# Optimization experiments

Measured on AMD Instinct MI355X. Metric: run time of the kernel, lower is better.

## Reference

```python
import jax, jax.numpy as jnp
import numpy as np

B, C, L = 4, 512, 2048
CI = 512          # inter_channels (must equal num_heads*head_dim)
H, D = 8, 64      # num_heads, head_dim = C // H
EPS = 1e-5        # BatchNorm1d eps


def setup_inputs() -> dict:
    key = jax.random.key(0)
    ks = jax.random.split(key, 9)
    s_in = 1.0 / np.sqrt(C)
    s_ci = 1.0 / np.sqrt(CI)
    return {
        "x": jax.random.normal(ks[0], (B, C, L), dtype=jnp.float32),
        "g_w": jax.random.uniform(ks[1], (CI, C), jnp.float32, -s_in, s_in),
        "g_b": jax.random.uniform(ks[2], (CI,), jnp.float32, -s_in, s_in),
        "theta_w": jax.random.uniform(ks[3], (CI, C), jnp.float32, -s_in, s_in),
        "theta_b": jax.random.uniform(ks[4], (CI,), jnp.float32, -s_in, s_in),
        "phi_w": jax.random.uniform(ks[5], (CI, C), jnp.float32, -s_in, s_in),
        "phi_b": jax.random.uniform(ks[6], (CI,), jnp.float32, -s_in, s_in),
        "w_w": jax.random.uniform(ks[7], (C, CI), jnp.float32, -s_ci, s_ci),
        "w_b": jax.random.uniform(ks[8], (C,), jnp.float32, -s_ci, s_ci),
        # BN affine params (torch inits them to 0, which zeroes the output;
        # use random values so the reference output / grads are non-trivial)
        "bn_gamma": jax.random.normal(jax.random.fold_in(key, 10), (C,), jnp.float32),
        "bn_beta": jax.random.normal(jax.random.fold_in(key, 11), (C,), jnp.float32),
    }


def _conv1x1(w, b, x):
    # x: [B, Cin, L], w: [Cout, Cin] -> [B, Cout, L]
    return jnp.einsum("oc,bcl->bol", w, x) + b[None, :, None]


def reference(x, g_w, g_b, theta_w, theta_b, phi_w, phi_b, w_w, w_b, bn_gamma, bn_beta):
    b, _, l = x.shape
    # 1x1 conv projections, split into heads: [B, H, D, L]
    g_x = _conv1x1(g_w, g_b, x).reshape(b, H, D, l).transpose(0, 1, 3, 2)      # [B,H,L,D]
    theta_x = _conv1x1(theta_w, theta_b, x).reshape(b, H, D, l).transpose(0, 1, 3, 2)  # [B,H,L,D]
    phi_x = _conv1x1(phi_w, phi_b, x).reshape(b, H, D, l)                       # [B,H,D,L]

    scale = 1.0 / jnp.sqrt(jnp.asarray(D, dtype=x.dtype))
    scores = jnp.einsum("bhqd,bhdk->bhqk", theta_x, phi_x) * scale  # [B,H,L,L]
    attn = jax.nn.softmax(scores, axis=-1)
    y = jnp.einsum("bhqk,bhkd->bhqd", attn, g_x)                    # [B,H,L,D]
    y = y.transpose(0, 1, 3, 2).reshape(b, CI, l)                   # [B,CI,L]

    # W: 1x1 conv + BatchNorm1d (training mode, biased batch stats)
    wy = _conv1x1(w_w, w_b, y)                                      # [B,C,L]
    mean = jnp.mean(wy, axis=(0, 2), keepdims=True)
    var = jnp.mean((wy - mean) ** 2, axis=(0, 2), keepdims=True)
    wy_hat = (wy - mean) * jax.lax.rsqrt(var + EPS)
    return wy_hat * bn_gamma[None, :, None] + bn_beta[None, :, None]
```

## Files before the change

### kernel.cpp

```cpp
#include <hip/hip_runtime.h>

constexpr int Bn = 4, Cn = 512, Ln = 2048, CIn = 512, Hn = 8, Dn = 64;
constexpr int COn = 3 * CIn;

typedef unsigned short u16;
typedef unsigned int u32;
typedef __attribute__((ext_vector_type(8))) short bfrag;
typedef __attribute__((ext_vector_type(4))) float facc;

#define SCF 0.180336879f

__device__ __forceinline__ facc mfma16(bfrag a, bfrag b, facc c) {
  return __builtin_amdgcn_mfma_f32_16x16x32_bf16(a, b, c, 0, 0, 0);
}

__device__ __forceinline__ void async16(const void* g, void* l) {
  __builtin_amdgcn_global_load_lds((const __attribute__((address_space(1))) void*)g,
                                   (__attribute__((address_space(3))) void*)l, 16, 0, 0);
}

__device__ __forceinline__ u16 f2bf(float x) {
  union { float f; u32 u; } v; v.f = x;
  u32 r = v.u + 0x7FFFu + ((v.u >> 16) & 1u);
  return (u16)(r >> 16);
}

__device__ __forceinline__ u16 f2bf_fast(float x) {
  union { float f; u32 u; } v; v.f = x;
  return (u16)((v.u + 0x8000u) >> 16);
}

__device__ __forceinline__ u32 pkbf(float lof, float hif) {
  union { float f; u32 u; } a, b; a.f = lof; b.f = hif;
  return __builtin_amdgcn_perm(b.u + 0x8000u, a.u + 0x8000u, 0x07060302u);
}

__device__ __forceinline__ float bflo(u32 u) { return __uint_as_float(u << 16); }
__device__ __forceinline__ float bfhi(u32 u) { return __uint_as_float(u & 0xFFFF0000u); }

__device__ __forceinline__ bfrag fr8(const u16* base, int row, int gi) {
  return *(const bfrag*)&base[row * 64 + ((gi ^ (row & 7)) * 8)];
}

__global__ void k_misc(const float* __restrict__ x, const float* __restrict__ gw,
                       const float* __restrict__ tw, const float* __restrict__ pw,
                       const float* __restrict__ ww, u16* __restrict__ xT,
                       u16* __restrict__ Wcat, u16* __restrict__ Ww,
                       float* __restrict__ stats) {
  int b = blockIdx.z;
  if (b == 4) {
    int i = (blockIdx.y * 64 + blockIdx.x) * 256 + threadIdx.x;
    if (i < CIn * Cn) {
      Wcat[i]                = f2bf(tw[i] * SCF);
      Wcat[CIn * Cn + i]     = f2bf(pw[i]);
      Wcat[2 * CIn * Cn + i] = f2bf(gw[i]);
      Ww[i]                  = f2bf(ww[i]);
    }
    if (i < 2 * Cn) stats[i] = 0.f;
    return;
  }
  __shared__ float tile[32][33];
  int l0 = blockIdx.x * 32, c0 = blockIdx.y * 32;
  int tx = threadIdx.x & 31, ty = threadIdx.x >> 5;
  const float* xb = x + (size_t)b * Cn * Ln;
  for (int k = 0; k < 4; k++)
    tile[ty + k * 8][tx] = xb[(size_t)(c0 + ty + k * 8) * Ln + l0 + tx];
  __syncthreads();
  u16* xtb = xT + (size_t)b * Ln * Cn;
  int cc = (threadIdx.x & 15) * 2, r0 = threadIdx.x >> 4;
  for (int k = 0; k < 2; k++) {
    int ll = r0 + k * 16;
    u32 pk = pkbf(tile[cc][ll], tile[cc + 1][ll]);
    *(u32*)&xtb[(size_t)(l0 + ll) * Cn + c0 + cc] = pk;
  }
}

__device__ __forceinline__ void stage128x32(const u16* g, int K, int k0, u16* lds,
                                            int w, int l) {
  int gsw = ((l & 3) ^ ((l >> 3) & 3)) * 8;
  for (int jj = 0; jj < 2; jj++) {
    int j = w * 2 + jj;
    const u16* ga = g + (size_t)(j * 16 + (l >> 2)) * K + k0 + gsw;
    async16(ga, (char*)lds + j * 1024 + l * 16);
  }
}

__device__ __forceinline__ void gemm_core(const u16* A, const u16* Bt, int K,
                                          u16* As, u16* Bs, facc acc[4][4],
                                          int w, int l) {
  int quad = l >> 4, lo = l & 15;
  int mw = (w >> 1) * 64, nw = (w & 1) * 64;
  int rsw = (lo >> 1) & 3;
  for (int k0 = 0; k0 < K; k0 += 32) {
    stage128x32(A, K, k0, As, w, l);
    stage128x32(Bt, K, k0, Bs, w, l);
    __syncthreads();
    bfrag af[4], bfv[4];
    for (int mi = 0; mi < 4; mi++)
      af[mi] = *(const bfrag*)&As[(mw + mi * 16 + lo) * 32 + ((quad ^ rsw) * 8)];
    for (int ni = 0; ni < 4; ni++)
      bfv[ni] = *(const bfrag*)&Bs[(nw + ni * 16 + lo) * 32 + ((quad ^ rsw) * 8)];
    for (int mi = 0; mi < 4; mi++)
      for (int ni = 0; ni < 4; ni++)
        acc[mi][ni] = mfma16(af[mi], bfv[ni], acc[mi][ni]);
    __syncthreads();
  }
}

__device__ __forceinline__ void gemm_core64(const u16* A, const u16* Bt, int K,
                                            u16* As, u16* Bs, facc acc[2][4],
                                            int w, int l) {
  int quad = l >> 4, lo = l & 15;
  int mw = (w >> 1) * 32, nw = (w & 1) * 64;
  int rsw = (lo >> 1) & 3;
  int gsw = ((l & 3) ^ ((l >> 3) & 3)) * 8;
  for (int k0 = 0; k0 < K; k0 += 32) {
    async16(A + (size_t)(w * 16 + (l >> 2)) * K + k0 + gsw, (char*)As + w * 1024 + l * 16);
    stage128x32(Bt, K, k0, Bs, w, l);
    __syncthreads();
    bfrag af[2], bfv[4];
    for (int mi = 0; mi < 2; mi++)
      af[mi] = *(const bfrag*)&As[(mw + mi * 16 + lo) * 32 + ((quad ^ rsw) * 8)];
    for (int ni = 0; ni < 4; ni++)
      bfv[ni] = *(const bfrag*)&Bs[(nw + ni * 16 + lo) * 32 + ((quad ^ rsw) * 8)];
    for (int mi = 0; mi < 2; mi++)
      for (int ni = 0; ni < 4; ni++)
        acc[mi][ni] = mfma16(af[mi], bfv[ni], acc[mi][ni]);
    __syncthreads();
  }
}

__global__ __launch_bounds__(256) void k_proj(
    const u16* __restrict__ Wcat, const u16* __restrict__ xT,
    const float* __restrict__ tb, const float* __restrict__ pb,
    const float* __restrict__ gb, u16* __restrict__ Q, u16* __restrict__ Kb,
    u16* __restrict__ Vt) {
  __shared__ __align__(16) u16 As[128 * 32];
  __shared__ __align__(16) u16 Bs[128 * 32];
  int w = threadIdx.x >> 6, l = threadIdx.x & 63;
  int quad = l >> 4, lo = l & 15;
  int m0 = blockIdx.y * 128, n0 = blockIdx.x * 128, b = blockIdx.z;
  facc acc[4][4] = {};
  gemm_core(Wcat + (size_t)m0 * Cn, xT + ((size_t)b * Ln + n0) * Cn, Cn, As, Bs, acc, w, l);
  int mw = (w >> 1) * 64, nw = (w & 1) * 64;
  int chunk = m0 >> 9;
  for (int mi = 0; mi < 4; mi++) {
    int mo = (m0 + mw + mi * 16) & 511;
    int hh = mo >> 6;
    int db = (mo & 63) + quad * 4;
    int bi = mo + quad * 4;
    if (chunk < 2) {
      const float* bias = (chunk == 0) ? tb : pb;
      float bs = (chunk == 0) ? SCF : 1.0f;
      u16* dst0 = ((chunk == 0) ? Q : Kb) + (size_t)(b * Hn + hh) * Ln * 64 + db;
      float b0 = bias[bi] * bs, b1 = bias[bi + 1] * bs;
      float b2 = bias[bi + 2] * bs, b3 = bias[bi + 3] * bs;
      for (int ni = 0; ni < 4; ni++) {
        int lcol = n0 + nw + ni * 16 + lo;
        facc a = acc[mi][ni];
        uint2 pk;
        pk.x = pkbf(a[0] + b0, a[1] + b1);
        pk.y = pkbf(a[2] + b2, a[3] + b3);
        *(uint2*)(dst0 + (size_t)lcol * 64) = pk;
      }
    } else {
      for (int ni = 0; ni < 4; ni++) {
        int lcol = n0 + nw + ni * 16 + lo;
        facc a = acc[mi][ni];
        for (int r = 0; r < 4; r++)
          Vt[((size_t)(b * Hn + hh) * Dn + db + r) * Ln + lcol] = f2bf_fast(a[r] + gb[bi + r]);
      }
    }
  }
}

__global__ __launch_bounds__(256, 2) void k_attn(
    const u16* __restrict__ Q, const u16* __restrict__ Kb,
    const u16* __restrict__ Vt, u16* __restrict__ Opart,
    float* __restrict__ lpart) {
  __shared__ __align__(16) u16 lds[24576];
  u16* Ks = lds;
  u16* Vs = lds + 8192;
  u16* QPs = lds + 16384;
  int w = threadIdx.x >> 6, l = threadIdx.x & 63;
  int quad = l >> 4, lo = l & 15;
  int q0 = blockIdx.x * 128, h = blockIdx.y >> 1, split = blockIdx.y & 1, b = blockIdx.z;
  size_t bh = (size_t)b * Hn + h;
  const u16* Qg = Q + bh * Ln * 64;
  const u16* Kg = Kb + bh * Ln * 64 + (size_t)split * 1024 * 64;
  const u16* Vg = Vt + bh * (size_t)Dn * Ln + split * 1024;

  int rin = l >> 3;
  int gg = ((l & 7) ^ rin) * 8;

  for (int jj = 0; jj < 4; jj++) {
    int j = w * 4 + jj;
    async16(Qg + (size_t)(q0 + j * 8 + rin) * 64 + gg, (char*)QPs + j * 1024 + l * 16);
  }
  for (int jj = 0; jj < 2; jj++) {
    int j = w * 2 + jj;
    async16(Kg + (size_t)(j * 8 + rin) * 64 + gg, (char*)Ks + j * 1024 + l * 16);
    async16(Vg + (size_t)(j * 8 + rin) * Ln + gg, (char*)Vs + j * 1024 + l * 16);
  }
  __syncthreads();
  bfrag qf[2][2];
  for (int s = 0; s < 2; s++)
    for (int c = 0; c < 2; c++)
      qf[s][c] = fr8(QPs, w * 32 + s * 16 + lo, c * 4 + quad);

  facc o[2][4] = {};
  float l_i[2] = {0.f, 0.f};

  for (int t = 0; t < 16; t++) {
    const u16* Kc = Ks + (t & 1) * 4096;
    const u16* Vc = Vs + (t & 1) * 4096;
    if (t < 15) {
      int nb = (~t & 1) * 4096;
      int kbase = (t + 1) * 64;
      for (int jj = 0; jj < 2; jj++) {
        int j = w * 2 + jj;
        async16(Kg + (size_t)(kbase + j * 8 + rin) * 64 + gg,
                (char*)(Ks + nb) + j * 1024 + l * 16);
        async16(Vg + (size_t)(j * 8 + rin) * Ln + kbase + gg,
                (char*)(Vs + nb) + j * 1024 + l * 16);
      }
    }
    for (int ni = 0; ni < 4; ni++) {
      bfrag kf0 = fr8(Kc, ni * 16 + lo, quad);
      bfrag kf1 = fr8(Kc, ni * 16 + lo, 4 + quad);
      for (int s = 0; s < 2; s++) {
        facc z = {};
        facc stv = mfma16(kf1, qf[s][1], mfma16(kf0, qf[s][0], z));
        float p0 = __builtin_amdgcn_exp2f(stv[0]);
        float p1 = __builtin_amdgcn_exp2f(stv[1]);
        float p2 = __builtin_amdgcn_exp2f(stv[2]);
        float p3 = __builtin_amdgcn_exp2f(stv[3]);
        l_i[s] += (p0 + p1) + (p2 + p3);
        int row = w * 32 + s * 16 + lo;
        uint2 pk;
        pk.x = pkbf(p0, p1);
        pk.y = pkbf(p2, p3);
        int gi = ni * 2 + (quad >> 1);
        *(uint2*)&QPs[row * 64 + ((gi ^ (row & 7)) * 8) + (quad & 1) * 4] = pk;
      }
    }
    bfrag pb2[2][2];
    for (int s = 0; s < 2; s++)
      for (int c = 0; c < 2; c++)
        pb2[s][c] = fr8(QPs, w * 32 + s * 16 + lo, c * 4 + quad);
    for (int mi = 0; mi < 4; mi++) {
      bfrag vf0 = fr8(Vc, mi * 16 + lo, quad);
      bfrag vf1 = fr8(Vc, mi * 16 + lo, 4 + quad);
      for (int s = 0; s < 2; s++)
        o[s][mi] = mfma16(vf1, pb2[s][1], mfma16(vf0, pb2[s][0], o[s][mi]));
    }
    __syncthreads();
  }
  int sb = split * 32 + (int)bh;
  for (int s = 0; s < 2; s++) {
    float lt = l_i[s];
    lt += __shfl_xor(lt, 16);
    lt += __shfl_xor(lt, 32);
    int q = q0 + w * 32 + s * 16 + lo;
    u16* dst = Opart + ((size_t)sb * Ln + q) * 64;
    for (int mi = 0; mi < 4; mi++) {
      uint2 pk;
      pk.x = pkbf(o[s][mi][0], o[s][mi][1]);
      pk.y = pkbf(o[s][mi][2], o[s][mi][3]);
      *(uint2*)(dst + mi * 16 + quad * 4) = pk;
    }
    if (quad == 0) lpart[(size_t)sb * Ln + q] = lt;
  }
}

__global__ void k_comb(const u16* __restrict__ Opart, const float* __restrict__ lpart,
                       u16* __restrict__ yT) {
  int i = blockIdx.x * 256 + threadIdx.x;
  int bhq = i >> 3, d0 = (i & 7) * 8;
  int bh = bhq >> 11, q = bhq & 2047;
  const u16* o1 = Opart + ((size_t)bh * Ln + q) * 64 + d0;
  const u16* o2 = o1 + (size_t)32 * Ln * 64;
  float inv = 1.0f / (lpart[bhq] + lpart[65536 + bhq]);
  uint4 a = *(const uint4*)o1, c = *(const uint4*)o2;
  uint4 r;
  r.x = pkbf((bflo(a.x) + bflo(c.x)) * inv, (bfhi(a.x) + bfhi(c.x)) * inv);
  r.y = pkbf((bflo(a.y) + bflo(c.y)) * inv, (bfhi(a.y) + bfhi(c.y)) * inv);
  r.z = pkbf((bflo(a.z) + bflo(c.z)) * inv, (bfhi(a.z) + bfhi(c.z)) * inv);
  r.w = pkbf((bflo(a.w) + bflo(c.w)) * inv, (bfhi(a.w) + bfhi(c.w)) * inv);
  int b = bh >> 3, h = bh & 7;
  *(uint4*)(yT + ((size_t)b * Ln + q) * CIn + h * 64 + d0) = r;
}

__global__ __launch_bounds__(256) void k_wgemm(
    const u16* __restrict__ Ww, const u16* __restrict__ yT,
    const float* __restrict__ wb, u16* __restrict__ wy,
    float* __restrict__ stats) {
  __shared__ __align__(16) u16 As[64 * 32];
  __shared__ __align__(16) u16 Bs[128 * 32];
  int w = threadIdx.x >> 6, l = threadIdx.x & 63;
  int quad = l >> 4, lo = l & 15;
  int m0 = blockIdx.y * 64, n0 = blockIdx.x * 128, b = blockIdx.z;
  facc acc[2][4] = {};
  gemm_core64(Ww + (size_t)m0 * CIn, yT + ((size_t)b * Ln + n0) * CIn, CIn, As, Bs, acc, w, l);
  int mw = (w >> 1) * 32, nw = (w & 1) * 64;
  for (int mi = 0; mi < 2; mi++) {
    int cb = m0 + mw + mi * 16 + quad * 4;
    for (int r = 0; r < 4; r++) {
      float bias = wb[cb + r];
      float s = 0.f, q = 0.f;
      for (int ni = 0; ni < 4; ni++) {
        float v = acc[mi][ni][r] + bias;
        wy[((size_t)b * Cn + cb + r) * Ln + n0 + nw + ni * 16 + lo] = f2bf_fast(v);
        s += v; q += v * v;
      }
      for (int mask = 1; mask < 16; mask <<= 1) {
        s += __shfl_xor(s, mask);
        q += __shfl_xor(q, mask);
      }
      if (lo == 0) {
        atomicAdd(&stats[cb + r], s);
        atomicAdd(&stats[Cn + cb + r], q);
      }
    }
  }
}

__global__ void k_bn(const u16* __restrict__ wy, const float* __restrict__ stats,
                     const float* __restrict__ gam, const float* __restrict__ bet,
                     float* __restrict__ out) {
  int i = blockIdx.x * 256 + threadIdx.x;
  size_t idx = (size_t)i * 8;
  int c = (int)((idx >> 11) & (Cn - 1));
  const float invN = 1.f / (Bn * Ln);
  float mean = stats[c] * invN;
  float var = stats[Cn + c] * invN - mean * mean;
  float scl = gam[c] * rsqrtf(var + 1e-5f);
  float sh = bet[c] - mean * scl;
  uint4 v = *(const uint4*)(wy + idx);
  float4 o0, o1;
  o0.x = bflo(v.x) * scl + sh; o0.y = bfhi(v.x) * scl + sh;
  o0.z = bflo(v.y) * scl + sh; o0.w = bfhi(v.y) * scl + sh;
  o1.x = bflo(v.z) * scl + sh; o1.y = bfhi(v.z) * scl + sh;
  o1.z = bflo(v.w) * scl + sh; o1.w = bfhi(v.w) * scl + sh;
  *(float4*)(out + idx) = o0;
  *(float4*)(out + idx + 4) = o1;
}

extern "C" void kernel_launch(void* const* d_in, const int* in_sizes, int n_in,
                              void* d_out, int out_size, void* d_ws, size_t ws_size,
                              hipStream_t stream) {
  const float* x   = (const float*)d_in[0];
  const float* g_w = (const float*)d_in[1];
  const float* g_b = (const float*)d_in[2];
  const float* t_w = (const float*)d_in[3];
  const float* t_b = (const float*)d_in[4];
  const float* p_w = (const float*)d_in[5];
  const float* p_b = (const float*)d_in[6];
  const float* w_w = (const float*)d_in[7];
  const float* w_b = (const float*)d_in[8];
  const float* gam = (const float*)d_in[9];
  const float* bet = (const float*)d_in[10];
  float* out = (float*)d_out;

  char* ws = (char*)d_ws;
  size_t off = 0;
  auto alloc = [&](size_t bytes) {
    char* p = ws + off; off += (bytes + 255) & ~(size_t)255; return p;
  };
  u16*  xT   = (u16*)alloc((size_t)Bn * Ln * Cn * 2);
  u16*  Wcat = (u16*)alloc((size_t)COn * Cn * 2);
  u16*  Ww   = (u16*)alloc((size_t)Cn * CIn * 2);
  u16*  Qb   = (u16*)alloc((size_t)Bn * Hn * Ln * Dn * 2);
  u16*  Kb   = (u16*)alloc((size_t)Bn * Hn * Ln * Dn * 2);
  u16*  Vt   = (u16*)alloc((size_t)Bn * Hn * Dn * Ln * 2);
  u16*  yT   = (u16*)alloc((size_t)Bn * Ln * CIn * 2);
  size_t opart_bytes = (size_t)2 * 32 * Ln * 64 * 2;
  u16*  Opart = (u16*)alloc(opart_bytes);
  u16*  wy    = Opart;
  float* lpart = (float*)alloc((size_t)2 * 32 * Ln * 4);
  float* st  = (float*)alloc(2 * Cn * 4);
  if (ws_size < off) return;

  k_misc<<<dim3(64, 16, 5), 256, 0, stream>>>(x, g_w, t_w, p_w, w_w, xT, Wcat, Ww, st);
  k_proj<<<dim3(16, 12, 4), 256, 0, stream>>>(Wcat, xT, t_b, p_b, g_b, Qb, Kb, Vt);
  k_attn<<<dim3(16, 16, 4), 256, 0, stream>>>(Qb, Kb, Vt, Opart, lpart);
  k_comb<<<dim3(2048), 256, 0, stream>>>(Opart, lpart, yT);
  k_wgemm<<<dim3(16, 8, 4), 256, 0, stream>>>(Ww, yT, w_b, wy, st);
  k_bn<<<dim3(2048), 256, 0, stream>>>(wy, st, gam, bet, out);
}
```

Baseline: 195.5 us.

## Fuse split-KV combine into attention via atomic counter, halve KV tile size

The attention kernel now processes 32-key tiles instead of 64, halving LDS use so four blocks can be resident per CU, as the new launch bound requests. The separate combine kernel is removed. Each block writes its partial output, and whichever of the two split blocks finishes last, detected with a global atomic counter and fences, reads the other split's partial and writes the normalized result to yT. This saves a kernel launch and one pass over the partials, at the cost of doubling the loop iterations and barriers and adding fence and atomic overhead.

```diff
diff --git a/kernel.cpp b/kernel.cpp
--- a/kernel.cpp
+++ b/kernel.cpp
@@ -40,6 +40,9 @@
 
 __device__ __forceinline__ bfrag fr8(const u16* base, int row, int gi) {
   return *(const bfrag*)&base[row * 64 + ((gi ^ (row & 7)) * 8)];
+}
+__device__ __forceinline__ bfrag fr4(const u16* base, int row, int gi) {
+  return *(const bfrag*)&base[row * 32 + ((gi ^ (row & 3)) * 8)];
 }
 
 __global__ void k_misc(const float* __restrict__ x, const float* __restrict__ gw,
@@ -56,7 +59,7 @@
       Wcat[2 * CIn * Cn + i] = f2bf(gw[i]);
       Ww[i]                  = f2bf(ww[i]);
     }
-    if (i < 2 * Cn) stats[i] = 0.f;
+    if (i < 2 * Cn + 512) stats[i] = 0.f;
     return;
   }
   __shared__ float tile[32][33];
@@ -174,14 +177,15 @@
   }
 }
 
-__global__ __launch_bounds__(256, 2) void k_attn(
+__global__ __launch_bounds__(256, 4) void k_attn(
     const u16* __restrict__ Q, const u16* __restrict__ Kb,
     const u16* __restrict__ Vt, u16* __restrict__ Opart,
-    float* __restrict__ lpart) {
-  __shared__ __align__(16) u16 lds[24576];
+    float* __restrict__ lpart, int* __restrict__ cnt, u16* __restrict__ yT) {
+  __shared__ __align__(16) u16 lds[16384];
+  __shared__ int sOld;
   u16* Ks = lds;
-  u16* Vs = lds + 8192;
-  u16* QPs = lds + 16384;
+  u16* Vs = lds + 4096;
+  u16* QPs = lds + 8192;
   int w = threadIdx.x >> 6, l = threadIdx.x & 63;
   int quad = l >> 4, lo = l & 15;
   int q0 = blockIdx.x * 128, h = blockIdx.y >> 1, split = blockIdx.y & 1, b = blockIdx.z;
@@ -192,16 +196,14 @@
 
   int rin = l >> 3;
   int gg = ((l & 7) ^ rin) * 8;
+  int ggv = ((l & 3) ^ ((l >> 2) & 3)) * 8;
 
   for (int jj = 0; jj < 4; jj++) {
     int j = w * 4 + jj;
     async16(Qg + (size_t)(q0 + j * 8 + rin) * 64 + gg, (char*)QPs + j * 1024 + l * 16);
   }
-  for (int jj = 0; jj < 2; jj++) {
-    int j = w * 2 + jj;
-    async16(Kg + (size_t)(j * 8 + rin) * 64 + gg, (char*)Ks + j * 1024 + l * 16);
-    async16(Vg + (size_t)(j * 8 + rin) * Ln + gg, (char*)Vs + j * 1024 + l * 16);
-  }
+  async16(Kg + (size_t)(w * 8 + rin) * 64 + gg, (char*)Ks + w * 1024 + l * 16);
+  async16(Vg + (size_t)(w * 16 + (l >> 2)) * Ln + ggv, (char*)Vs + w * 1024 + l * 16);
   __syncthreads();
   bfrag qf[2][2];
   for (int s = 0; s < 2; s++)
@@ -211,21 +213,18 @@
   facc o[2][4] = {};
   float l_i[2] = {0.f, 0.f};
 
-  for (int t = 0; t < 16; t++) {
-    const u16* Kc = Ks + (t & 1) * 4096;
-    const u16* Vc = Vs + (t & 1) * 4096;
-    if (t < 15) {
-      int nb = (~t & 1) * 4096;
-      int kbase = (t + 1) * 64;
-      for (int jj = 0; jj < 2; jj++) {
-        int j = w * 2 + jj;
-        async16(Kg + (size_t)(kbase + j * 8 + rin) * 64 + gg,
-                (char*)(Ks + nb) + j * 1024 + l * 16);
-        async16(Vg + (size_t)(j * 8 + rin) * Ln + kbase + gg,
-                (char*)(Vs + nb) + j * 1024 + l * 16);
-      }
-    }
-    for (int ni = 0; ni < 4; ni++) {
+  for (int t = 0; t < 32; t++) {
+    const u16* Kc = Ks + (t & 1) * 2048;
+    const u16* Vc = Vs + (t & 1) * 2048;
+    if (t < 31) {
+      int nb = (~t & 1) * 2048;
+      int kbase = (t + 1) * 32;
+      async16(Kg + (size_t)(kbase + w * 8 + rin) * 64 + gg,
+              (char*)(Ks + nb) + w * 1024 + l * 16);
+      async16(Vg + (size_t)(w * 16 + (l >> 2)) * Ln + kbase + ggv,
+              (char*)(Vs + nb) + w * 1024 + l * 16);
+    }
+    for (int ni = 0; ni < 2; ni++) {
       bfrag kf0 = fr8(Kc, ni * 16 + lo, quad);
       bfrag kf1 = fr8(Kc, ni * 16 + lo, 4 + quad);
       for (int s = 0; s < 2; s++) {
@@ -244,23 +243,24 @@
         *(uint2*)&QPs[row * 64 + ((gi ^ (row & 7)) * 8) + (quad & 1) * 4] = pk;
       }
     }
-    bfrag pb2[2][2];
+    bfrag pb2[2];
     for (int s = 0; s < 2; s++)
-      for (int c = 0; c < 2; c++)
-        pb2[s][c] = fr8(QPs, w * 32 + s * 16 + lo, c * 4 + quad);
+      pb2[s] = fr8(QPs, w * 32 + s * 16 + lo, quad);
     for (int mi = 0; mi < 4; mi++) {
-      bfrag vf0 = fr8(Vc, mi * 16 + lo, quad);
-      bfrag vf1 = fr8(Vc, mi * 16 + lo, 4 + quad);
+      bfrag vf = fr4(Vc, mi * 16 + lo, quad);
       for (int s = 0; s < 2; s++)
-        o[s][mi] = mfma16(vf1, pb2[s][1], mfma16(vf0, pb2[s][0], o[s][mi]));
-    }
-    __syncthreads();
-  }
+        o[s][mi] = mfma16(vf, pb2[s], o[s][mi]);
+    }
+    __syncthreads();
+  }
+
   int sb = split * 32 + (int)bh;
+  float lt[2];
   for (int s = 0; s < 2; s++) {
-    float lt = l_i[s];
-    lt += __shfl_xor(lt, 16);
-    lt += __shfl_xor(lt, 32);
+    float v = l_i[s];
+    v += __shfl_xor(v, 16);
+    v += __shfl_xor(v, 32);
+    lt[s] = v;
     int q = q0 + w * 32 + s * 16 + lo;
     u16* dst = Opart + ((size_t)sb * Ln + q) * 64;
     for (int mi = 0; mi < 4; mi++) {
@@ -269,26 +269,29 @@
       pk.y = pkbf(o[s][mi][2], o[s][mi][3]);
       *(uint2*)(dst + mi * 16 + quad * 4) = pk;
     }
-    if (quad == 0) lpart[(size_t)sb * Ln + q] = lt;
-  }
-}
-
-__global__ void k_comb(const u16* __restrict__ Opart, const float* __restrict__ lpart,
-                       u16* __restrict__ yT) {
-  int i = blockIdx.x * 256 + threadIdx.x;
-  int bhq = i >> 3, d0 = (i & 7) * 8;
-  int bh = bhq >> 11, q = bhq & 2047;
-  const u16* o1 = Opart + ((size_t)bh * Ln + q) * 64 + d0;
-  const u16* o2 = o1 + (size_t)32 * Ln * 64;
-  float inv = 1.0f / (lpart[bhq] + lpart[65536 + bhq]);
-  uint4 a = *(const uint4*)o1, c = *(const uint4*)o2;
-  uint4 r;
-  r.x = pkbf((bflo(a.x) + bflo(c.x)) * inv, (bfhi(a.x) + bfhi(c.x)) * inv);
-  r.y = pkbf((bflo(a.y) + bflo(c.y)) * inv, (bfhi(a.y) + bfhi(c.y)) * inv);
-  r.z = pkbf((bflo(a.z) + bflo(c.z)) * inv, (bfhi(a.z) + bfhi(c.z)) * inv);
-  r.w = pkbf((bflo(a.w) + bflo(c.w)) * inv, (bfhi(a.w) + bfhi(c.w)) * inv);
-  int b = bh >> 3, h = bh & 7;
-  *(uint4*)(yT + ((size_t)b * Ln + q) * CIn + h * 64 + d0) = r;
+    if (quad == 0) lpart[(size_t)sb * Ln + q] = lt[s];
+  }
+  __threadfence();
+  __syncthreads();
+  if (threadIdx.x == 0)
+    sOld = atomicAdd(cnt + ((int)bh * 16 + blockIdx.x), 1);
+  __syncthreads();
+  if (sOld == 0) return;
+  __threadfence();
+  int sbo = (1 - split) * 32 + (int)bh;
+  for (int s = 0; s < 2; s++) {
+    int q = q0 + w * 32 + s * 16 + lo;
+    const u16* osrc = Opart + ((size_t)sbo * Ln + q) * 64;
+    float inv = 1.0f / (lt[s] + lpart[(size_t)sbo * Ln + q]);
+    u16* dst = yT + ((size_t)b * Ln + q) * CIn + h * 64;
+    for (int mi = 0; mi < 4; mi++) {
+      uint2 ov = *(const uint2*)(osrc + mi * 16 + quad * 4);
+      uint2 pk;
+      pk.x = pkbf((o[s][mi][0] + bflo(ov.x)) * inv, (o[s][mi][1] + bfhi(ov.x)) * inv);
+      pk.y = pkbf((o[s][mi][2] + bflo(ov.y)) * inv, (o[s][mi][3] + bfhi(ov.y)) * inv);
+      *(uint2*)(dst + mi * 16 + quad * 4) = pk;
+    }
+  }
 }
 
 __global__ __launch_bounds__(256) void k_wgemm(
@@ -378,13 +381,13 @@
   u16*  Opart = (u16*)alloc(opart_bytes);
   u16*  wy    = Opart;
   float* lpart = (float*)alloc((size_t)2 * 32 * Ln * 4);
-  float* st  = (float*)alloc(2 * Cn * 4);
+  float* st  = (float*)alloc((2 * Cn + 512) * 4);
+  int*  cnt  = (int*)(st + 2 * Cn);
   if (ws_size < off) return;
 
   k_misc<<<dim3(64, 16, 5), 256, 0, stream>>>(x, g_w, t_w, p_w, w_w, xT, Wcat, Ww, st);
   k_proj<<<dim3(16, 12, 4), 256, 0, stream>>>(Wcat, xT, t_b, p_b, g_b, Qb, Kb, Vt);
-  k_attn<<<dim3(16, 16, 4), 256, 0, stream>>>(Qb, Kb, Vt, Opart, lpart);
-  k_comb<<<dim3(2048), 256, 0, stream>>>(Opart, lpart, yT);
+  k_attn<<<dim3(16, 16, 4), 256, 0, stream>>>(Qb, Kb, Vt, Opart, lpart, cnt, yT);
   k_wgemm<<<dim3(16, 8, 4), 256, 0, stream>>>(Ww, yT, w_b, wy, st);
   k_bn<<<dim3(2048), 256, 0, stream>>>(wy, st, gam, bet, out);
 }
```

After: 382.9 us. +95.8%, slower.

## Fuse split-KV combine into W-GEMM loader and vectorize V-transpose stores

Applied to the files above, without the earlier changes.

Removes the separate combine kernel by having the W-projection GEMM read both attention partial outputs and their softmax denominators, normalize them, and write bf16 directly into its shared-memory B tile. This drops one launch and the yT round trip through global memory. The cost is synchronous global loads in the GEMM main loop in place of async LDS loads, with the combine work repeated across the 8 M-tile blocks. Separately, the V projection swaps the MFMA operands so each lane holds consecutive sequence positions and can emit packed 8-byte stores instead of scalar 2-byte scattered writes. wy is given its own buffer instead of aliasing Opart.

```diff
diff --git a/kernel.cpp b/kernel.cpp
--- a/kernel.cpp
+++ b/kernel.cpp
@@ -85,6 +85,7 @@
   }
 }
 
+template <int SWAP>
 __device__ __forceinline__ void gemm_core(const u16* A, const u16* Bt, int K,
                                           u16* As, u16* Bs, facc acc[4][4],
                                           int w, int l) {
@@ -102,30 +103,8 @@
       bfv[ni] = *(const bfrag*)&Bs[(nw + ni * 16 + lo) * 32 + ((quad ^ rsw) * 8)];
     for (int mi = 0; mi < 4; mi++)
       for (int ni = 0; ni < 4; ni++)
-        acc[mi][ni] = mfma16(af[mi], bfv[ni], acc[mi][ni]);
-    __syncthreads();
-  }
-}
-
-__device__ __forceinline__ void gemm_core64(const u16* A, const u16* Bt, int K,
-                                            u16* As, u16* Bs, facc acc[2][4],
-                                            int w, int l) {
-  int quad = l >> 4, lo = l & 15;
-  int mw = (w >> 1) * 32, nw = (w & 1) * 64;
-  int rsw = (lo >> 1) & 3;
-  int gsw = ((l & 3) ^ ((l >> 3) & 3)) * 8;
-  for (int k0 = 0; k0 < K; k0 += 32) {
-    async16(A + (size_t)(w * 16 + (l >> 2)) * K + k0 + gsw, (char*)As + w * 1024 + l * 16);
-    stage128x32(Bt, K, k0, Bs, w, l);
-    __syncthreads();
-    bfrag af[2], bfv[4];
-    for (int mi = 0; mi < 2; mi++)
-      af[mi] = *(const bfrag*)&As[(mw + mi * 16 + lo) * 32 + ((quad ^ rsw) * 8)];
-    for (int ni = 0; ni < 4; ni++)
-      bfv[ni] = *(const bfrag*)&Bs[(nw + ni * 16 + lo) * 32 + ((quad ^ rsw) * 8)];
-    for (int mi = 0; mi < 2; mi++)
-      for (int ni = 0; ni < 4; ni++)
-        acc[mi][ni] = mfma16(af[mi], bfv[ni], acc[mi][ni]);
+        acc[mi][ni] = SWAP ? mfma16(bfv[ni], af[mi], acc[mi][ni])
+                           : mfma16(af[mi], bfv[ni], acc[mi][ni]);
     __syncthreads();
   }
 }
@@ -140,18 +119,20 @@
   int w = threadIdx.x >> 6, l = threadIdx.x & 63;
   int quad = l >> 4, lo = l & 15;
   int m0 = blockIdx.y * 128, n0 = blockIdx.x * 128, b = blockIdx.z;
+  int chunk = m0 >> 9;
   facc acc[4][4] = {};
-  gemm_core(Wcat + (size_t)m0 * Cn, xT + ((size_t)b * Ln + n0) * Cn, Cn, As, Bs, acc, w, l);
+  const u16* Ap = Wcat + (size_t)m0 * Cn;
+  const u16* Bp = xT + ((size_t)b * Ln + n0) * Cn;
   int mw = (w >> 1) * 64, nw = (w & 1) * 64;
-  int chunk = m0 >> 9;
-  for (int mi = 0; mi < 4; mi++) {
-    int mo = (m0 + mw + mi * 16) & 511;
-    int hh = mo >> 6;
-    int db = (mo & 63) + quad * 4;
-    int bi = mo + quad * 4;
-    if (chunk < 2) {
-      const float* bias = (chunk == 0) ? tb : pb;
-      float bs = (chunk == 0) ? SCF : 1.0f;
+  if (chunk < 2) {
+    gemm_core<0>(Ap, Bp, Cn, As, Bs, acc, w, l);
+    const float* bias = (chunk == 0) ? tb : pb;
+    float bs = (chunk == 0) ? SCF : 1.0f;
+    for (int mi = 0; mi < 4; mi++) {
+      int mo = (m0 + mw + mi * 16) & 511;
+      int hh = mo >> 6;
+      int db = (mo & 63) + quad * 4;
+      int bi = mo + quad * 4;
       u16* dst0 = ((chunk == 0) ? Q : Kb) + (size_t)(b * Hn + hh) * Ln * 64 + db;
       float b0 = bias[bi] * bs, b1 = bias[bi + 1] * bs;
       float b2 = bias[bi + 2] * bs, b3 = bias[bi + 3] * bs;
@@ -163,12 +144,21 @@
         pk.y = pkbf(a[2] + b2, a[3] + b3);
         *(uint2*)(dst0 + (size_t)lcol * 64) = pk;
       }
-    } else {
+    }
+  } else {
+    gemm_core<1>(Ap, Bp, Cn, As, Bs, acc, w, l);
+    for (int mi = 0; mi < 4; mi++) {
+      int ch = (m0 + mw + mi * 16 + lo) & 511;
+      int hh = ch >> 6, d = ch & 63;
+      float bias = gb[ch];
+      u16* dst0 = Vt + ((size_t)(b * Hn + hh) * Dn + d) * Ln;
       for (int ni = 0; ni < 4; ni++) {
-        int lcol = n0 + nw + ni * 16 + lo;
+        int l0 = n0 + nw + ni * 16 + quad * 4;
         facc a = acc[mi][ni];
-        for (int r = 0; r < 4; r++)
-          Vt[((size_t)(b * Hn + hh) * Dn + db + r) * Ln + lcol] = f2bf_fast(a[r] + gb[bi + r]);
+        uint2 pk;
+        pk.x = pkbf(a[0] + bias, a[1] + bias);
+        pk.y = pkbf(a[2] + bias, a[3] + bias);
+        *(uint2*)(dst0 + l0) = pk;
       }
     }
   }
@@ -273,36 +263,58 @@
   }
 }
 
-__global__ void k_comb(const u16* __restrict__ Opart, const float* __restrict__ lpart,
-                       u16* __restrict__ yT) {
-  int i = blockIdx.x * 256 + threadIdx.x;
-  int bhq = i >> 3, d0 = (i & 7) * 8;
-  int bh = bhq >> 11, q = bhq & 2047;
-  const u16* o1 = Opart + ((size_t)bh * Ln + q) * 64 + d0;
-  const u16* o2 = o1 + (size_t)32 * Ln * 64;
-  float inv = 1.0f / (lpart[bhq] + lpart[65536 + bhq]);
-  uint4 a = *(const uint4*)o1, c = *(const uint4*)o2;
-  uint4 r;
-  r.x = pkbf((bflo(a.x) + bflo(c.x)) * inv, (bfhi(a.x) + bfhi(c.x)) * inv);
-  r.y = pkbf((bflo(a.y) + bflo(c.y)) * inv, (bfhi(a.y) + bfhi(c.y)) * inv);
-  r.z = pkbf((bflo(a.z) + bflo(c.z)) * inv, (bfhi(a.z) + bfhi(c.z)) * inv);
-  r.w = pkbf((bflo(a.w) + bflo(c.w)) * inv, (bfhi(a.w) + bfhi(c.w)) * inv);
-  int b = bh >> 3, h = bh & 7;
-  *(uint4*)(yT + ((size_t)b * Ln + q) * CIn + h * 64 + d0) = r;
-}
-
 __global__ __launch_bounds__(256) void k_wgemm(
-    const u16* __restrict__ Ww, const u16* __restrict__ yT,
-    const float* __restrict__ wb, u16* __restrict__ wy,
-    float* __restrict__ stats) {
+    const u16* __restrict__ Ww, const u16* __restrict__ Opart,
+    const float* __restrict__ lpart, const float* __restrict__ wb,
+    u16* __restrict__ wy, float* __restrict__ stats) {
   __shared__ __align__(16) u16 As[64 * 32];
   __shared__ __align__(16) u16 Bs[128 * 32];
-  int w = threadIdx.x >> 6, l = threadIdx.x & 63;
+  int tid = threadIdx.x;
+  int w = tid >> 6, l = tid & 63;
   int quad = l >> 4, lo = l & 15;
   int m0 = blockIdx.y * 64, n0 = blockIdx.x * 128, b = blockIdx.z;
+  const u16* A = Ww + (size_t)m0 * CIn;
   facc acc[2][4] = {};
-  gemm_core64(Ww + (size_t)m0 * CIn, yT + ((size_t)b * Ln + n0) * CIn, CIn, As, Bs, acc, w, l);
+  int gsw = ((l & 3) ^ ((l >> 3) & 3)) * 8;
+  int rsw = (lo >> 1) & 3;
   int mw = (w >> 1) * 32, nw = (w & 1) * 64;
+  int row = tid >> 1;
+  int rg = n0 + row;
+  int half = tid & 1;
+  int ssw = (row >> 1) & 3;
+  for (int k0 = 0; k0 < CIn; k0 += 32) {
+    async16(A + (size_t)(w * 16 + (l >> 2)) * CIn + k0 + gsw,
+            (char*)As + w * 1024 + l * 16);
+    int h = k0 >> 6;
+    int sb0 = b * 8 + h;
+    const u16* p1 = Opart + ((size_t)sb0 * Ln + rg) * 64 + (k0 & 63) + half * 16;
+    const u16* p2 = p1 + (size_t)32 * Ln * 64;
+    float inv = 1.0f / (lpart[(size_t)sb0 * Ln + rg] +
+                        lpart[(size_t)(sb0 + 32) * Ln + rg]);
+    uint4 a1 = *(const uint4*)p1, c1 = *(const uint4*)p2;
+    uint4 a2 = *(const uint4*)(p1 + 8), c2 = *(const uint4*)(p2 + 8);
+    uint4 r1, r2;
+    r1.x = pkbf((bflo(a1.x) + bflo(c1.x)) * inv, (bfhi(a1.x) + bfhi(c1.x)) * inv);
+    r1.y = pkbf((bflo(a1.y) + bflo(c1.y)) * inv, (bfhi(a1.y) + bfhi(c1.y)) * inv);
+    r1.z = pkbf((bflo(a1.z) + bflo(c1.z)) * inv, (bfhi(a1.z) + bfhi(c1.z)) * inv);
+    r1.w = pkbf((bflo(a1.w) + bflo(c1.w)) * inv, (bfhi(a1.w) + bfhi(c1.w)) * inv);
+    r2.x = pkbf((bflo(a2.x) + bflo(c2.x)) * inv, (bfhi(a2.x) + bfhi(c2.x)) * inv);
+    r2.y = pkbf((bflo(a2.y) + bflo(c2.y)) * inv, (bfhi(a2.y) + bfhi(c2.y)) * inv);
+    r2.z = pkbf((bflo(a2.z) + bflo(c2.z)) * inv, (bfhi(a2.z) + bfhi(c2.z)) * inv);
+    r2.w = pkbf((bflo(a2.w) + bflo(c2.w)) * inv, (bfhi(a2.w) + bfhi(c2.w)) * inv);
+    *(uint4*)&Bs[row * 32 + (((half * 2) ^ ssw) * 8)] = r1;
+    *(uint4*)&Bs[row * 32 + (((half * 2 + 1) ^ ssw) * 8)] = r2;
+    __syncthreads();
+    bfrag af[2], bfv[4];
+    for (int mi = 0; mi < 2; mi++)
+      af[mi] = *(const bfrag*)&As[(mw + mi * 16 + lo) * 32 + ((quad ^ rsw) * 8)];
+    for (int ni = 0; ni < 4; ni++)
+      bfv[ni] = *(const bfrag*)&Bs[(nw + ni * 16 + lo) * 32 + ((quad ^ rsw) * 8)];
+    for (int mi = 0; mi < 2; mi++)
+      for (int ni = 0; ni < 4; ni++)
+        acc[mi][ni] = mfma16(af[mi], bfv[ni], acc[mi][ni]);
+    __syncthreads();
+  }
   for (int mi = 0; mi < 2; mi++) {
     int cb = m0 + mw + mi * 16 + quad * 4;
     for (int r = 0; r < 4; r++) {
@@ -373,18 +385,15 @@
   u16*  Qb   = (u16*)alloc((size_t)Bn * Hn * Ln * Dn * 2);
   u16*  Kb   = (u16*)alloc((size_t)Bn * Hn * Ln * Dn * 2);
   u16*  Vt   = (u16*)alloc((size_t)Bn * Hn * Dn * Ln * 2);
-  u16*  yT   = (u16*)alloc((size_t)Bn * Ln * CIn * 2);
-  size_t opart_bytes = (size_t)2 * 32 * Ln * 64 * 2;
-  u16*  Opart = (u16*)alloc(opart_bytes);
-  u16*  wy    = Opart;
+  u16*  Opart = (u16*)alloc((size_t)2 * 32 * Ln * 64 * 2);
   float* lpart = (float*)alloc((size_t)2 * 32 * Ln * 4);
+  u16*  wy   = (u16*)alloc((size_t)Bn * Cn * Ln * 2);
   float* st  = (float*)alloc(2 * Cn * 4);
   if (ws_size < off) return;
 
   k_misc<<<dim3(64, 16, 5), 256, 0, stream>>>(x, g_w, t_w, p_w, w_w, xT, Wcat, Ww, st);
   k_proj<<<dim3(16, 12, 4), 256, 0, stream>>>(Wcat, xT, t_b, p_b, g_b, Qb, Kb, Vt);
   k_attn<<<dim3(16, 16, 4), 256, 0, stream>>>(Qb, Kb, Vt, Opart, lpart);
-  k_comb<<<dim3(2048), 256, 0, stream>>>(Opart, lpart, yT);
-  k_wgemm<<<dim3(16, 8, 4), 256, 0, stream>>>(Ww, yT, w_b, wy, st);
+  k_wgemm<<<dim3(16, 8, 4), 256, 0, stream>>>(Ww, Opart, lpart, w_b, wy, st);
   k_bn<<<dim3(2048), 256, 0, stream>>>(wy, st, gam, bet, out);
 }
```

Measured after the change: 196.1 us. Within noise of the previous version (+0.3%).

## Split attention keys three ways and vectorize transposed V projection stores

Applied to the files above, without the earlier changes.

The attention kernel now splits the 32 key tiles into three chunks (11/11/10) instead of two halves. This raises the grid from 1024 to 1536 blocks so the MI355X's CUs are better filled, and the combine kernel sums three partials. The V projection swaps the MFMA operand order so each lane holds contiguous sequence positions, allowing packed 8-byte stores into Vt instead of scattered 2-byte stores. The workspace is rearranged so yT and wy reuse the Q/K buffers, which keeps memory use in check with the larger partial buffers, at the cost of more partial-output traffic in the combine step.

```diff
diff --git a/kernel.cpp b/kernel.cpp
--- a/kernel.cpp
+++ b/kernel.cpp
@@ -85,6 +85,7 @@
   }
 }
 
+template <int SWAP>
 __device__ __forceinline__ void gemm_core(const u16* A, const u16* Bt, int K,
                                           u16* As, u16* Bs, facc acc[4][4],
                                           int w, int l) {
@@ -102,7 +103,8 @@
       bfv[ni] = *(const bfrag*)&Bs[(nw + ni * 16 + lo) * 32 + ((quad ^ rsw) * 8)];
     for (int mi = 0; mi < 4; mi++)
       for (int ni = 0; ni < 4; ni++)
-        acc[mi][ni] = mfma16(af[mi], bfv[ni], acc[mi][ni]);
+        acc[mi][ni] = SWAP ? mfma16(bfv[ni], af[mi], acc[mi][ni])
+                           : mfma16(af[mi], bfv[ni], acc[mi][ni]);
     __syncthreads();
   }
 }
@@ -140,18 +142,20 @@
   int w = threadIdx.x >> 6, l = threadIdx.x & 63;
   int quad = l >> 4, lo = l & 15;
   int m0 = blockIdx.y * 128, n0 = blockIdx.x * 128, b = blockIdx.z;
+  int chunk = m0 >> 9;
   facc acc[4][4] = {};
-  gemm_core(Wcat + (size_t)m0 * Cn, xT + ((size_t)b * Ln + n0) * Cn, Cn, As, Bs, acc, w, l);
+  const u16* Ap = Wcat + (size_t)m0 * Cn;
+  const u16* Bp = xT + ((size_t)b * Ln + n0) * Cn;
   int mw = (w >> 1) * 64, nw = (w & 1) * 64;
-  int chunk = m0 >> 9;
-  for (int mi = 0; mi < 4; mi++) {
-    int mo = (m0 + mw + mi * 16) & 511;
-    int hh = mo >> 6;
-    int db = (mo & 63) + quad * 4;
-    int bi = mo + quad * 4;
-    if (chunk < 2) {
-      const float* bias = (chunk == 0) ? tb : pb;
-      float bs = (chunk == 0) ? SCF : 1.0f;
+  if (chunk < 2) {
+    gemm_core<0>(Ap, Bp, Cn, As, Bs, acc, w, l);
+    const float* bias = (chunk == 0) ? tb : pb;
+    float bs = (chunk == 0) ? SCF : 1.0f;
+    for (int mi = 0; mi < 4; mi++) {
+      int mo = (m0 + mw + mi * 16) & 511;
+      int hh = mo >> 6;
+      int db = (mo & 63) + quad * 4;
+      int bi = mo + quad * 4;
       u16* dst0 = ((chunk == 0) ? Q : Kb) + (size_t)(b * Hn + hh) * Ln * 64 + db;
       float b0 = bias[bi] * bs, b1 = bias[bi + 1] * bs;
       float b2 = bias[bi + 2] * bs, b3 = bias[bi + 3] * bs;
@@ -163,12 +167,21 @@
         pk.y = pkbf(a[2] + b2, a[3] + b3);
         *(uint2*)(dst0 + (size_t)lcol * 64) = pk;
       }
-    } else {
+    }
+  } else {
+    gemm_core<1>(Ap, Bp, Cn, As, Bs, acc, w, l);
+    for (int mi = 0; mi < 4; mi++) {
+      int ch = (m0 + mw + mi * 16 + lo) & 511;
+      int hh = ch >> 6, d = ch & 63;
+      float bias = gb[ch];
+      u16* dst0 = Vt + ((size_t)(b * Hn + hh) * Dn + d) * Ln;
       for (int ni = 0; ni < 4; ni++) {
-        int lcol = n0 + nw + ni * 16 + lo;
+        int l0 = n0 + nw + ni * 16 + quad * 4;
         facc a = acc[mi][ni];
-        for (int r = 0; r < 4; r++)
-          Vt[((size_t)(b * Hn + hh) * Dn + db + r) * Ln + lcol] = f2bf_fast(a[r] + gb[bi + r]);
+        uint2 pk;
+        pk.x = pkbf(a[0] + bias, a[1] + bias);
+        pk.y = pkbf(a[2] + bias, a[3] + bias);
+        *(uint2*)(dst0 + l0) = pk;
       }
     }
   }
@@ -184,11 +197,14 @@
   u16* QPs = lds + 16384;
   int w = threadIdx.x >> 6, l = threadIdx.x & 63;
   int quad = l >> 4, lo = l & 15;
-  int q0 = blockIdx.x * 128, h = blockIdx.y >> 1, split = blockIdx.y & 1, b = blockIdx.z;
+  int q0 = blockIdx.x * 128, b = blockIdx.z;
+  int h = blockIdx.y / 3, split = blockIdx.y - h * 3;
+  int ts = split * 11;
+  int nt = (split == 2) ? 10 : 11;
   size_t bh = (size_t)b * Hn + h;
   const u16* Qg = Q + bh * Ln * 64;
-  const u16* Kg = Kb + bh * Ln * 64 + (size_t)split * 1024 * 64;
-  const u16* Vg = Vt + bh * (size_t)Dn * Ln + split * 1024;
+  const u16* Kg = Kb + bh * Ln * 64 + (size_t)ts * 4096;
+  const u16* Vg = Vt + bh * (size_t)Dn * Ln + ts * 64;
 
   int rin = l >> 3;
   int gg = ((l & 7) ^ rin) * 8;
@@ -211,10 +227,10 @@
   facc o[2][4] = {};
   float l_i[2] = {0.f, 0.f};
 
-  for (int t = 0; t < 16; t++) {
+  for (int t = 0; t < nt; t++) {
     const u16* Kc = Ks + (t & 1) * 4096;
     const u16* Vc = Vs + (t & 1) * 4096;
-    if (t < 15) {
+    if (t < nt - 1) {
       int nb = (~t & 1) * 4096;
       int kbase = (t + 1) * 64;
       for (int jj = 0; jj < 2; jj++) {
@@ -280,13 +296,18 @@
   int bh = bhq >> 11, q = bhq & 2047;
   const u16* o1 = Opart + ((size_t)bh * Ln + q) * 64 + d0;
   const u16* o2 = o1 + (size_t)32 * Ln * 64;
-  float inv = 1.0f / (lpart[bhq] + lpart[65536 + bhq]);
-  uint4 a = *(const uint4*)o1, c = *(const uint4*)o2;
+  const u16* o3 = o2 + (size_t)32 * Ln * 64;
+  float inv = 1.0f / (lpart[bhq] + lpart[65536 + bhq] + lpart[131072 + bhq]);
+  uint4 a = *(const uint4*)o1, c = *(const uint4*)o2, e = *(const uint4*)o3;
   uint4 r;
-  r.x = pkbf((bflo(a.x) + bflo(c.x)) * inv, (bfhi(a.x) + bfhi(c.x)) * inv);
-  r.y = pkbf((bflo(a.y) + bflo(c.y)) * inv, (bfhi(a.y) + bfhi(c.y)) * inv);
-  r.z = pkbf((bflo(a.z) + bflo(c.z)) * inv, (bfhi(a.z) + bfhi(c.z)) * inv);
-  r.w = pkbf((bflo(a.w) + bflo(c.w)) * inv, (bfhi(a.w) + bfhi(c.w)) * inv);
+  r.x = pkbf((bflo(a.x) + bflo(c.x) + bflo(e.x)) * inv,
+             (bfhi(a.x) + bfhi(c.x) + bfhi(e.x)) * inv);
+  r.y = pkbf((bflo(a.y) + bflo(c.y) + bflo(e.y)) * inv,
+             (bfhi(a.y) + bfhi(c.y) + bfhi(e.y)) * inv);
+  r.z = pkbf((bflo(a.z) + bflo(c.z) + bflo(e.z)) * inv,
+             (bfhi(a.z) + bfhi(c.z) + bfhi(e.z)) * inv);
+  r.w = pkbf((bflo(a.w) + bflo(c.w) + bflo(e.w)) * inv,
+             (bfhi(a.w) + bfhi(c.w) + bfhi(e.w)) * inv);
   int b = bh >> 3, h = bh & 7;
   *(uint4*)(yT + ((size_t)b * Ln + q) * CIn + h * 64 + d0) = r;
 }
@@ -373,17 +394,16 @@
   u16*  Qb   = (u16*)alloc((size_t)Bn * Hn * Ln * Dn * 2);
   u16*  Kb   = (u16*)alloc((size_t)Bn * Hn * Ln * Dn * 2);
   u16*  Vt   = (u16*)alloc((size_t)Bn * Hn * Dn * Ln * 2);
-  u16*  yT   = (u16*)alloc((size_t)Bn * Ln * CIn * 2);
-  size_t opart_bytes = (size_t)2 * 32 * Ln * 64 * 2;
-  u16*  Opart = (u16*)alloc(opart_bytes);
-  u16*  wy    = Opart;
-  float* lpart = (float*)alloc((size_t)2 * 32 * Ln * 4);
+  u16*  Opart = (u16*)alloc((size_t)3 * 32 * Ln * 64 * 2);
+  float* lpart = (float*)alloc((size_t)3 * 32 * Ln * 4);
   float* st  = (float*)alloc(2 * Cn * 4);
+  u16* yT = Kb;
+  u16* wy = Qb;
   if (ws_size < off) return;
 
   k_misc<<<dim3(64, 16, 5), 256, 0, stream>>>(x, g_w, t_w, p_w, w_w, xT, Wcat, Ww, st);
   k_proj<<<dim3(16, 12, 4), 256, 0, stream>>>(Wcat, xT, t_b, p_b, g_b, Qb, Kb, Vt);
-  k_attn<<<dim3(16, 16, 4), 256, 0, stream>>>(Qb, Kb, Vt, Opart, lpart);
+  k_attn<<<dim3(16, 24, 4), 256, 0, stream>>>(Qb, Kb, Vt, Opart, lpart);
   k_comb<<<dim3(2048), 256, 0, stream>>>(Opart, lpart, yT);
   k_wgemm<<<dim3(16, 8, 4), 256, 0, stream>>>(Ww, yT, w_b, wy, st);
   k_bn<<<dim3(2048), 256, 0, stream>>>(wy, st, gam, bet, out);
```

New measurement: 191.3 us. 1.02x faster.
